# Kernel optimization log

Hardware: AMD Instinct MI355X
Metric: run time of the kernel (lower is better)

Reference implementation:

```python
import jax, jax.numpy as jnp
import numpy as np

N = 50000
E = 800000
IN_DIM = 128
H1 = 512
H2 = 300
OUT_DIM = 10
EPS = 1e-5


def setup_inputs() -> dict:
    key = jax.random.key(0)
    ks = jax.random.split(key, 12)
    x = jax.random.normal(ks[0], (N, IN_DIM), dtype=jnp.float32)
    edge_index = jax.random.randint(ks[1], (2, E), 0, N, dtype=jnp.int64)
    edge_weight = jax.random.uniform(ks[2], (E,), dtype=jnp.float32)
    def glorot(k, fan_in, fan_out):
        lim = np.sqrt(6.0 / (fan_in + fan_out)).astype(np.float32)
        return jax.random.uniform(k, (fan_in, fan_out), jnp.float32, -lim, lim)
    return {
        "x": x,
        "edge_index": edge_index,
        "edge_weight": edge_weight,
        "W1": glorot(ks[3], IN_DIM, H1), "b1": jnp.zeros((H1,), jnp.float32),
        "g1": jnp.ones((H1,), jnp.float32), "beta1": jnp.zeros((H1,), jnp.float32),
        "W2": glorot(ks[4], H1, H2), "b2": jnp.zeros((H2,), jnp.float32),
        "g2": jnp.ones((H2,), jnp.float32), "beta2": jnp.zeros((H2,), jnp.float32),
        "Wl": glorot(ks[5], H2, OUT_DIM), "bl": jnp.zeros((OUT_DIM,), jnp.float32),
    }


def _gcn_norm(edge_index, edge_weight, n):
    # add self loops (fill value 1.0), then symmetric normalization (PyG gcn_norm)
    si = jnp.arange(n, dtype=edge_index.dtype)
    row = jnp.concatenate([edge_index[0], si])  # source
    col = jnp.concatenate([edge_index[1], si])  # target
    w = jnp.concatenate([edge_weight, jnp.ones((n,), edge_weight.dtype)])
    deg = jax.ops.segment_sum(w, col, num_segments=n)
    dis = jnp.where(deg > 0, jax.lax.rsqrt(deg), 0.0)
    return row, col, dis[row] * w * dis[col]


def _propagate(h, row, col, norm, n):
    # gather source rows, weight, scatter-add into targets
    return jax.ops.segment_sum(h[row] * norm[:, None], col, num_segments=n)


def _batchnorm(h, g, beta):
    mean = jnp.mean(h, axis=0)
    var = jnp.mean(jnp.square(h - mean), axis=0)  # biased var (torch BN)
    return (h - mean) * jax.lax.rsqrt(var + EPS) * g + beta


def reference(x, edge_index, edge_weight, W1, b1, g1, beta1,
              W2, b2, g2, beta2, Wl, bl):
    n = x.shape[0]
    row, col, norm = _gcn_norm(edge_index, edge_weight, n)
    # layer 1: aggregate then transform (== GCNConv's lin-then-propagate math)
    h = _propagate(x, row, col, norm, n) @ W1 + b1
    h = jax.nn.relu(_batchnorm(h, g1, beta1))
    # layer 2: transform then aggregate
    h = _propagate(h @ W2, row, col, norm, n) + b2
    h = jax.nn.relu(_batchnorm(h, g2, beta2))
    # classifier head + log_softmax
    h = jax.nn.relu(h @ Wl + bl)
    return jax.nn.log_softmax(h, axis=1)
```

## Files before the change

### kernel.cpp

```cpp
#include <hip/hip_runtime.h>
#include <math.h>

namespace {

constexpr int kIn  = 128;
constexpr int kH1  = 512;
constexpr int kH2  = 300;
constexpr int kH2p = 304;
constexpr int kW2R = 384;
constexpr int kOut = 10;
constexpr float kEps = 1e-5f;

typedef __attribute__((ext_vector_type(8))) short bf16x8;
typedef __attribute__((ext_vector_type(4))) float f32x4;

__device__ __forceinline__ void atomAddF(float* p, float v) { unsafeAtomicAdd(p, v); }

__device__ __forceinline__ unsigned short f2bf(float f) {
  unsigned u = __builtin_bit_cast(unsigned, f);
  unsigned r = u + 0x7fffu + ((u >> 16) & 1u);
  return (unsigned short)(r >> 16);
}
__device__ __forceinline__ float bf2f(unsigned short h) {
  return __builtin_bit_cast(float, (unsigned)h << 16);
}
__device__ __forceinline__ float blo(unsigned u) { return __builtin_bit_cast(float, u << 16); }
__device__ __forceinline__ float bhi(unsigned u) { return __builtin_bit_cast(float, u & 0xffff0000u); }
__device__ __forceinline__ unsigned pk2(float a, float b) {
  return (unsigned)f2bf(a) | ((unsigned)f2bf(b) << 16);
}

__device__ __forceinline__ void gload16(const unsigned short* g, unsigned short* l) {
  __builtin_amdgcn_global_load_lds(
      (const __attribute__((address_space(1))) unsigned int*)g,
      (__attribute__((address_space(3))) unsigned int*)l, 16, 0, 0);
}

__device__ __forceinline__ void fma8(const uint4& q, float w, float* acc) {
  acc[0] = fmaf(blo(q.x), w, acc[0]);
  acc[1] = fmaf(bhi(q.x), w, acc[1]);
  acc[2] = fmaf(blo(q.y), w, acc[2]);
  acc[3] = fmaf(bhi(q.y), w, acc[3]);
  acc[4] = fmaf(blo(q.z), w, acc[4]);
  acc[5] = fmaf(bhi(q.z), w, acc[5]);
  acc[6] = fmaf(blo(q.w), w, acc[6]);
  acc[7] = fmaf(bhi(q.w), w, acc[7]);
}

__global__ void k_prep(float* __restrict__ deg, int* __restrict__ cnt,
                       const float* __restrict__ x, unsigned short* __restrict__ xbf,
                       float* __restrict__ st,
                       const float* __restrict__ W1, unsigned short* __restrict__ W1T,
                       const float* __restrict__ W2, unsigned short* __restrict__ W2T, int n) {
  int i = blockIdx.x * blockDim.x + threadIdx.x;
  if (i < n) { deg[i] = 1.0f; cnt[i] = 0; }
  if (i < 4096) st[i] = 0.f;
  if (i < kIn * kH1) {
    int nn = i / kIn, k = i - nn * kIn;
    W1T[i] = f2bf(W1[(size_t)k * kH1 + nn]);
  }
  if (i < kW2R * kH1) {
    int nn = i / kH1, k = i - nn * kH1;
    W2T[i] = (nn < kH2) ? f2bf(W2[(size_t)k * kH2 + nn]) : (unsigned short)0;
  }
  if (i < n * 16) {
    int node = i >> 4, g = i & 15;
    const float4* xp = reinterpret_cast<const float4*>(x + (size_t)node * kIn + g * 8);
    float4 v0 = xp[0], v1 = xp[1];
    uint4 o;
    o.x = pk2(v0.x, v0.y); o.y = pk2(v0.z, v0.w);
    o.z = pk2(v1.x, v1.y); o.w = pk2(v1.z, v1.w);
    reinterpret_cast<uint4*>(xbf)[i] = o;
  }
}

__global__ void k_deg_cnt(float* __restrict__ deg, int* __restrict__ cnt,
                          const int* __restrict__ ei, const float* __restrict__ w, int nE) {
  int i = blockIdx.x * blockDim.x + threadIdx.x;
  if (i < nE) {
    int c = ei[nE + i];
    atomAddF(&deg[c], w[i]);
    atomicAdd(&cnt[c], 1);
  }
}

__global__ void k_dis(float* __restrict__ deg, int n) {
  int i = blockIdx.x * blockDim.x + threadIdx.x;
  if (i < n) deg[i] = rsqrtf(deg[i]);
}

__global__ void k_scan_a(int* __restrict__ cnt, int* __restrict__ bsum, int n) {
  __shared__ int ws[4];
  int i = blockIdx.x * 256 + threadIdx.x;
  int lane = threadIdx.x & 63, wid = threadIdx.x >> 6;
  int v = (i < n) ? cnt[i] : 0;
  int s = v;
#pragma unroll
  for (int off = 1; off < 64; off <<= 1) {
    int t = __shfl_up(s, off);
    if (lane >= off) s += t;
  }
  if (lane == 63) ws[wid] = s;
  __syncthreads();
  int add = 0;
  if (wid > 0) add += ws[0];
  if (wid > 1) add += ws[1];
  if (wid > 2) add += ws[2];
  if (i < n) cnt[i] = s - v + add;
  if (threadIdx.x == 255) bsum[blockIdx.x] = add + s;
}

__global__ void k_scan_b(int* __restrict__ bsum, int nb) {
  __shared__ int ws[4];
  int i = threadIdx.x;
  int lane = i & 63, wid = i >> 6;
  int v = (i < nb) ? bsum[i] : 0;
  int s = v;
#pragma unroll
  for (int off = 1; off < 64; off <<= 1) {
    int t = __shfl_up(s, off);
    if (lane >= off) s += t;
  }
  if (lane == 63) ws[wid] = s;
  __syncthreads();
  int add = 0;
  if (wid > 0) add += ws[0];
  if (wid > 1) add += ws[1];
  if (wid > 2) add += ws[2];
  if (i < nb) bsum[i] = s - v + add;
}

__global__ void k_scan_c(int* __restrict__ cnt, const int* __restrict__ bsum, int n) {
  int i = blockIdx.x * 256 + threadIdx.x;
  if (i < n) cnt[i] += bsum[blockIdx.x];
}

__global__ void k_scatter(int* __restrict__ cnt, const int* __restrict__ ei,
                          const float* __restrict__ w, const float* __restrict__ dis,
                          uint2* __restrict__ pr, int nE) {
  int i = blockIdx.x * blockDim.x + threadIdx.x;
  if (i < nE) {
    int r = ei[i];
    int c = ei[nE + i];
    int pos = atomicAdd(&cnt[c], 1);
    float ww = dis[r] * w[i] * dis[c];
    pr[pos] = make_uint2((unsigned)r, __builtin_bit_cast(unsigned, ww));
  }
}

template<int NSQ>
__global__ void k_gather(const unsigned short* __restrict__ X, const int* __restrict__ endp,
                         const uint2* __restrict__ pr, const float* __restrict__ dis,
                         unsigned short* __restrict__ out, int n) {
  int tid = blockIdx.x * blockDim.x + threadIdx.x;
  int v = tid / NSQ;
  int s = tid - v * NSQ;
  if (v >= n) return;
  int beg = (v == 0) ? 0 : endp[v - 1];
  int end = endp[v];
  const uint4* Xr = reinterpret_cast<const uint4*>(X);
  float d = dis[v];
  float sw = d * d;
  float acc[8];
  {
    uint4 q = Xr[(size_t)v * NSQ + s];
    acc[0] = blo(q.x) * sw; acc[1] = bhi(q.x) * sw;
    acc[2] = blo(q.y) * sw; acc[3] = bhi(q.y) * sw;
    acc[4] = blo(q.z) * sw; acc[5] = bhi(q.z) * sw;
    acc[6] = blo(q.w) * sw; acc[7] = bhi(q.w) * sw;
  }
  int e = beg;
  for (; e + 4 <= end; e += 4) {
    uint2 p0 = pr[e], p1 = pr[e + 1], p2 = pr[e + 2], p3 = pr[e + 3];
    uint4 q0 = Xr[(size_t)p0.x * NSQ + s];
    uint4 q1 = Xr[(size_t)p1.x * NSQ + s];
    uint4 q2 = Xr[(size_t)p2.x * NSQ + s];
    uint4 q3 = Xr[(size_t)p3.x * NSQ + s];
    fma8(q0, __builtin_bit_cast(float, p0.y), acc);
    fma8(q1, __builtin_bit_cast(float, p1.y), acc);
    fma8(q2, __builtin_bit_cast(float, p2.y), acc);
    fma8(q3, __builtin_bit_cast(float, p3.y), acc);
  }
  for (; e < end; ++e) {
    uint2 p = pr[e];
    uint4 q = Xr[(size_t)p.x * NSQ + s];
    fma8(q, __builtin_bit_cast(float, p.y), acc);
  }
  uint4 o;
  o.x = pk2(acc[0], acc[1]);
  o.y = pk2(acc[2], acc[3]);
  o.z = pk2(acc[4], acc[5]);
  o.w = pk2(acc[6], acc[7]);
  reinterpret_cast<uint4*>(out)[(size_t)v * NSQ + s] = o;
}

__global__ __launch_bounds__(256) void k_gemm(const unsigned short* __restrict__ A,
    const unsigned short* __restrict__ BT, unsigned short* __restrict__ C,
    int M, int Nlog, int K, int ntiles, int nwg) {
  constexpr int BK = 64;
  __shared__ unsigned short lA[(BK / 8) * 128 * 8];
  __shared__ unsigned short lB[(BK / 8) * 128 * 8];

  int p = blockIdx.x;
  int xcd = p & 7, idx = p >> 3;
  int q8 = nwg >> 3, r8 = nwg & 7;
  int logical = (xcd < r8 ? xcd * (q8 + 1) : r8 * (q8 + 1) + (xcd - r8) * q8) + idx;
  const int nt = logical % ntiles;
  const int mt = logical / ntiles;
  const int m0 = mt * 128, n0 = nt * 128;

  const int tid = threadIdx.x, lane = tid & 63, wid = tid >> 6;
  const int wr = wid >> 1, wc = wid & 1;
  const int fr = lane & 15, fq = lane >> 4;

  int arow[4], brow[4], k8s[4];
#pragma unroll
  for (int j = 0; j < 4; ++j) {
    int g = tid + 256 * j;
    int row = g & 127;
    k8s[j] = g >> 7;
    int ar = m0 + row;
    arow[j] = (ar < M) ? ar : (M - 1);
    brow[j] = n0 + row;
  }

  f32x4 acc[4][4] = {};

  for (int k0 = 0; k0 < K; k0 += BK) {
    __syncthreads();
#pragma unroll
    for (int j = 0; j < 4; ++j) {
      int g = tid + 256 * j;
      gload16(A  + (size_t)arow[j] * K + k0 + k8s[j] * 8, &lA[g * 8]);
      gload16(BT + (size_t)brow[j] * K + k0 + k8s[j] * 8, &lB[g * 8]);
    }
    __syncthreads();
#pragma unroll
    for (int step = 0; step < 2; ++step) {
      bf16x8 af[4], bf[4];
#pragma unroll
      for (int m = 0; m < 4; ++m)
        af[m] = *reinterpret_cast<const bf16x8*>(
            &lA[(((step * 4 + fq) << 7) + wr * 64 + m * 16 + fr) * 8]);
#pragma unroll
      for (int nn = 0; nn < 4; ++nn)
        bf[nn] = *reinterpret_cast<const bf16x8*>(
            &lB[(((step * 4 + fq) << 7) + wc * 64 + nn * 16 + fr) * 8]);
#pragma unroll
      for (int m = 0; m < 4; ++m)
#pragma unroll
        for (int nn = 0; nn < 4; ++nn)
          acc[m][nn] = __builtin_amdgcn_mfma_f32_16x16x32_bf16(af[m], bf[nn], acc[m][nn], 0, 0, 0);
    }
  }

#pragma unroll
  for (int m = 0; m < 4; ++m) {
#pragma unroll
    for (int r = 0; r < 4; ++r) {
      int row = m0 + wr * 64 + m * 16 + fq * 4 + r;
      if (row >= M) continue;
#pragma unroll
      for (int nn = 0; nn < 4; ++nn) {
        int col = n0 + wc * 64 + nn * 16 + fr;
        if (col < Nlog)
          C[(size_t)row * Nlog + col] = f2bf(acc[m][nn][r]);
      }
    }
  }
}

template<int C>
__global__ __launch_bounds__(256) void k_bn_stats_co(const unsigned short* __restrict__ H,
                                                     float* __restrict__ s1, float* __restrict__ s2,
                                                     int n, int rpb) {
  constexpr int G = C / 8;
  __shared__ float redS[3][G][8];
  __shared__ float redQ[3][G][8];
  const int g = threadIdx.x & 63;
  const int rr = threadIdx.x >> 6;
  int r0 = blockIdx.x * rpb;
  int r1 = r0 + rpb; if (r1 > n) r1 = n;
  float sa[8] = {}, sq[8] = {};
  if (g < G) {
    for (int r = r0 + rr; r < r1; r += 4) {
      uint4 q = *reinterpret_cast<const uint4*>(H + (size_t)r * C + g * 8);
      float v[8] = {blo(q.x), bhi(q.x), blo(q.y), bhi(q.y),
                    blo(q.z), bhi(q.z), blo(q.w), bhi(q.w)};
#pragma unroll
      for (int j = 0; j < 8; ++j) {
        sa[j] += v[j];
        sq[j] = fmaf(v[j], v[j], sq[j]);
      }
    }
    if (rr > 0) {
#pragma unroll
      for (int j = 0; j < 8; ++j) {
        redS[rr - 1][g][j] = sa[j];
        redQ[rr - 1][g][j] = sq[j];
      }
    }
  }
  __syncthreads();
  if (rr == 0 && g < G) {
#pragma unroll
    for (int j = 0; j < 8; ++j) {
      float ts = sa[j] + redS[0][g][j] + redS[1][g][j] + redS[2][g][j];
      float tq = sq[j] + redQ[0][g][j] + redQ[1][g][j] + redQ[2][g][j];
      atomAddF(&s1[g * 8 + j], ts);
      atomAddF(&s2[g * 8 + j], tq);
    }
  }
}

__global__ void k_bn_finalize(const float* __restrict__ s1, const float* __restrict__ s2,
                              const float* __restrict__ g, const float* __restrict__ beta,
                              float* __restrict__ scale, float* __restrict__ shift,
                              int C, float invN) {
  int c = blockIdx.x * blockDim.x + threadIdx.x;
  if (c >= C) return;
  float mean = s1[c] * invN;
  float var = fmaxf(s2[c] * invN - mean * mean, 0.f);
  float sc = g[c] * rsqrtf(var + kEps);
  scale[c] = sc;
  shift[c] = beta[c] - mean * sc;
}

template<int C>
__global__ void k_bn_apply_relu_bf16(unsigned short* __restrict__ H,
                                     const float* __restrict__ scale,
                                     const float* __restrict__ shift, int total8) {
  int i = blockIdx.x * blockDim.x + threadIdx.x;
  if (i >= total8) return;
  uint4 q = reinterpret_cast<uint4*>(H)[i];
  int c = (i * 8) & (C - 1);
  unsigned w[4] = {q.x, q.y, q.z, q.w};
  unsigned o[4];
#pragma unroll
  for (int j = 0; j < 4; ++j) {
    float lo = blo(w[j]);
    float hi = bhi(w[j]);
    int cl = c + j * 2;
    lo = fmaxf(fmaf(lo, scale[cl],     shift[cl]),     0.f);
    hi = fmaxf(fmaf(hi, scale[cl + 1], shift[cl + 1]), 0.f);
    o[j] = pk2(lo, hi);
  }
  reinterpret_cast<uint4*>(H)[i] = make_uint4(o[0], o[1], o[2], o[3]);
}

__global__ __launch_bounds__(256) void k_head(const unsigned short* __restrict__ H,
    const float* __restrict__ scale, const float* __restrict__ shift,
    const float* __restrict__ Wl, const float* __restrict__ bl,
    float* __restrict__ out, int n) {
  __shared__ float sW[kH2 * kOut];
  __shared__ float sScale[kH2], sShift[kH2];
  for (int i = threadIdx.x; i < kH2 * kOut; i += blockDim.x) sW[i] = Wl[i];
  for (int i = threadIdx.x; i < kH2; i += blockDim.x) {
    sScale[i] = scale[i];
    sShift[i] = shift[i];
  }
  __syncthreads();
  float blv[kOut];
#pragma unroll
  for (int j = 0; j < kOut; ++j) blv[j] = bl[j];
  const int lane = threadIdx.x & 63;
  const int wid = (blockIdx.x * blockDim.x + threadIdx.x) >> 6;
  const int nw  = (gridDim.x * blockDim.x) >> 6;
  for (int node = wid; node < n; node += nw) {
    const unsigned short* hrow = H + (size_t)node * kH2p;
    float acc[kOut] = {};
    for (int k = lane; k < kH2; k += 64) {
      float v = fmaxf(fmaf(bf2f(hrow[k]), sScale[k], sShift[k]), 0.f);
      const float* wr = sW + k * kOut;
#pragma unroll
      for (int j = 0; j < kOut; ++j) acc[j] = fmaf(v, wr[j], acc[j]);
    }
#pragma unroll
    for (int j = 0; j < kOut; ++j) {
      float v = acc[j];
      for (int off = 32; off > 0; off >>= 1) v += __shfl_down(v, off);
      acc[j] = v;
    }
    if (lane == 0) {
      float vv[kOut], m = -1e30f;
#pragma unroll
      for (int j = 0; j < kOut; ++j) {
        vv[j] = fmaxf(acc[j] + blv[j], 0.f);
        m = fmaxf(m, vv[j]);
      }
      float s = 0.f;
#pragma unroll
      for (int j = 0; j < kOut; ++j) s += expf(vv[j] - m);
      float lse = m + logf(s);
      float* o = out + (size_t)node * kOut;
#pragma unroll
      for (int j = 0; j < kOut; ++j) o[j] = vv[j] - lse;
    }
  }
}

}

extern "C" void kernel_launch(void* const* d_in, const int* in_sizes, int n_in,
                              void* d_out, int out_size, void* d_ws, size_t ws_size,
                              hipStream_t stream) {
  const float* x   = (const float*)d_in[0];
  const int*   ei  = (const int*)d_in[1];
  const float* ew  = (const float*)d_in[2];
  const float* W1  = (const float*)d_in[3];
  const float* g1  = (const float*)d_in[5];
  const float* be1 = (const float*)d_in[6];
  const float* W2  = (const float*)d_in[7];
  const float* g2  = (const float*)d_in[9];
  const float* be2 = (const float*)d_in[10];
  const float* Wl  = (const float*)d_in[11];
  const float* bl  = (const float*)d_in[12];
  float* out = (float*)d_out;
  float* ws  = (float*)d_ws;

  const int n = in_sizes[0] / kIn;
  const int e = in_sizes[1] / 2;

  float* dis = ws;
  int*   cnt = (int*)(ws + 50048);
  uint2* pr  = (uint2*)(ws + 100096);
  float* st  = ws + 1700096;
  float* s1a = st,        *s2a = st + 512,  *sc1 = st + 1024, *sh1 = st + 1536;
  float* s1b = st + 2048, *s2b = st + 2560, *sc2 = st + 3072, *sh2 = st + 3584;
  int*   bsum = (int*)(ws + 1704192);
  unsigned short* xbf = (unsigned short*)(ws + 1704704);
  unsigned short* W1T = (unsigned short*)(ws + 4904704);
  unsigned short* W2T = (unsigned short*)(ws + 4937472);
  unsigned short* agg1 = (unsigned short*)(ws + 5035776);
  unsigned short* h1   = (unsigned short*)(ws + 8235776);
  unsigned short* t2   = (unsigned short*)(ws + 21035776);
  unsigned short* agg2 = (unsigned short*)(ws + 28635776);

  constexpr int TPB = 256;
  const int nb = (n + 255) / 256;
  const int rpb = (n + 255) / 256;

  k_prep<<<(n * 16 + TPB - 1) / TPB, TPB, 0, stream>>>(dis, cnt, x, xbf, st, W1, W1T, W2, W2T, n);
  k_deg_cnt<<<(e + TPB - 1) / TPB, TPB, 0, stream>>>(dis, cnt, ei, ew, e);
  k_dis<<<(n + TPB - 1) / TPB, TPB, 0, stream>>>(dis, n);
  k_scan_a<<<nb, 256, 0, stream>>>(cnt, bsum, n);
  k_scan_b<<<1, 256, 0, stream>>>(bsum, nb);
  k_scan_c<<<nb, 256, 0, stream>>>(cnt, bsum, n);
  k_scatter<<<(e + TPB - 1) / TPB, TPB, 0, stream>>>(cnt, ei, ew, dis, pr, e);

  const int mtiles = (n + 127) / 128;

  {
    int tot = n * (kIn / 8);
    k_gather<kIn / 8><<<(tot + TPB - 1) / TPB, TPB, 0, stream>>>(xbf, cnt, pr, dis, agg1, n);
  }
  {
    int ntiles = kH1 / 128;
    int nwg = mtiles * ntiles;
    k_gemm<<<nwg, 256, 0, stream>>>(agg1, W1T, h1, n, kH1, kIn, ntiles, nwg);
  }
  k_bn_stats_co<kH1><<<256, 256, 0, stream>>>(h1, s1a, s2a, n, rpb);
  k_bn_finalize<<<(kH1 + 255) / 256, 256, 0, stream>>>(s1a, s2a, g1, be1, sc1, sh1, kH1, 1.0f / n);
  k_bn_apply_relu_bf16<kH1><<<((n * (kH1 / 8)) + TPB - 1) / TPB, TPB, 0, stream>>>(
      h1, sc1, sh1, n * (kH1 / 8));

  {
    int ntiles = kW2R / 128;
    int nwg = mtiles * ntiles;
    k_gemm<<<nwg, 256, 0, stream>>>(h1, W2T, t2, n, kH2p, kH1, ntiles, nwg);
  }
  {
    int tot = n * (kH2p / 8);
    k_gather<kH2p / 8><<<(tot + TPB - 1) / TPB, TPB, 0, stream>>>(t2, cnt, pr, dis, agg2, n);
  }
  k_bn_stats_co<kH2p><<<256, 256, 0, stream>>>(agg2, s1b, s2b, n, rpb);
  k_bn_finalize<<<(kH2 + 255) / 256, 256, 0, stream>>>(s1b, s2b, g2, be2, sc2, sh2, kH2, 1.0f / n);

  k_head<<<1024, 256, 0, stream>>>(agg2, sc2, sh2, Wl, bl, out, n);
}
```

Measured before the change: 534.9 us.

## Fuse BN1 stats into GEMM epilogue, fold dis into scan, finalize into head

Layer-1 batchnorm sums and sums of squares are now accumulated in the GEMM epilogue, using shared-memory atomics per tile and then global atomics, in place of a separate stats kernel that re-read the whole h1 matrix. The rsqrt degree kernel is folded into the first scan pass, and the layer-2 BN finalize is computed inside the head kernel's shared-memory setup. This removes one full read of a large activation tensor and two small launches. In exchange it adds atomic contention on the 512 stat columns, and the stats are taken from fp32 accumulators instead of bf16-rounded values, so results can differ slightly.

```diff
diff --git a/kernel.cpp b/kernel.cpp
--- a/kernel.cpp
+++ b/kernel.cpp
@@ -84,15 +84,12 @@
   }
 }
 
-__global__ void k_dis(float* __restrict__ deg, int n) {
-  int i = blockIdx.x * blockDim.x + threadIdx.x;
-  if (i < n) deg[i] = rsqrtf(deg[i]);
-}
-
-__global__ void k_scan_a(int* __restrict__ cnt, int* __restrict__ bsum, int n) {
+__global__ void k_scan_a(int* __restrict__ cnt, int* __restrict__ bsum,
+                         float* __restrict__ deg, int n) {
   __shared__ int ws[4];
   int i = blockIdx.x * 256 + threadIdx.x;
   int lane = threadIdx.x & 63, wid = threadIdx.x >> 6;
+  if (i < n) deg[i] = rsqrtf(deg[i]);
   int v = (i < n) ? cnt[i] : 0;
   int s = v;
 #pragma unroll
@@ -194,12 +191,15 @@
   reinterpret_cast<uint4*>(out)[(size_t)v * NSQ + s] = o;
 }
 
+template<bool STATS>
 __global__ __launch_bounds__(256) void k_gemm(const unsigned short* __restrict__ A,
     const unsigned short* __restrict__ BT, unsigned short* __restrict__ C,
+    float* __restrict__ s1g, float* __restrict__ s2g,
     int M, int Nlog, int K, int ntiles, int nwg) {
   constexpr int BK = 64;
   __shared__ unsigned short lA[(BK / 8) * 128 * 8];
   __shared__ unsigned short lB[(BK / 8) * 128 * 8];
+  __shared__ float sS[128], sQ[128];
 
   int p = blockIdx.x;
   int xcd = p & 7, idx = p >> 3;
@@ -213,6 +213,10 @@
   const int wr = wid >> 1, wc = wid & 1;
   const int fr = lane & 15, fq = lane >> 4;
 
+  if constexpr (STATS) {
+    if (tid < 128) { sS[tid] = 0.f; sQ[tid] = 0.f; }
+  }
+
   int arow[4], brow[4], k8s[4];
 #pragma unroll
   for (int j = 0; j < 4; ++j) {
@@ -266,6 +270,36 @@
         if (col < Nlog)
           C[(size_t)row * Nlog + col] = f2bf(acc[m][nn][r]);
       }
+    }
+  }
+
+  if constexpr (STATS) {
+    float ps[4] = {}, pq[4] = {};
+#pragma unroll
+    for (int m = 0; m < 4; ++m) {
+#pragma unroll
+      for (int r = 0; r < 4; ++r) {
+        int row = m0 + wr * 64 + m * 16 + fq * 4 + r;
+        if (row < M) {
+#pragma unroll
+          for (int nn = 0; nn < 4; ++nn) {
+            float v = acc[m][nn][r];
+            ps[nn] += v;
+            pq[nn] = fmaf(v, v, pq[nn]);
+          }
+        }
+      }
+    }
+#pragma unroll
+    for (int nn = 0; nn < 4; ++nn) {
+      int cl = wc * 64 + nn * 16 + fr;
+      atomicAdd(&sS[cl], ps[nn]);
+      atomicAdd(&sQ[cl], pq[nn]);
+    }
+    __syncthreads();
+    if (tid < 128) {
+      atomAddF(&s1g[n0 + tid], sS[tid]);
+      atomAddF(&s2g[n0 + tid], sQ[tid]);
     }
   }
 }
@@ -349,15 +383,19 @@
 }
 
 __global__ __launch_bounds__(256) void k_head(const unsigned short* __restrict__ H,
-    const float* __restrict__ scale, const float* __restrict__ shift,
+    const float* __restrict__ s1, const float* __restrict__ s2,
+    const float* __restrict__ g2, const float* __restrict__ be2,
     const float* __restrict__ Wl, const float* __restrict__ bl,
-    float* __restrict__ out, int n) {
+    float* __restrict__ out, int n, float invN) {
   __shared__ float sW[kH2 * kOut];
   __shared__ float sScale[kH2], sShift[kH2];
   for (int i = threadIdx.x; i < kH2 * kOut; i += blockDim.x) sW[i] = Wl[i];
   for (int i = threadIdx.x; i < kH2; i += blockDim.x) {
-    sScale[i] = scale[i];
-    sShift[i] = shift[i];
+    float mean = s1[i] * invN;
+    float var = fmaxf(s2[i] * invN - mean * mean, 0.f);
+    float sc = g2[i] * rsqrtf(var + kEps);
+    sScale[i] = sc;
+    sShift[i] = be2[i] - mean * sc;
   }
   __syncthreads();
   float blv[kOut];
@@ -426,7 +464,7 @@
   uint2* pr  = (uint2*)(ws + 100096);
   float* st  = ws + 1700096;
   float* s1a = st,        *s2a = st + 512,  *sc1 = st + 1024, *sh1 = st + 1536;
-  float* s1b = st + 2048, *s2b = st + 2560, *sc2 = st + 3072, *sh2 = st + 3584;
+  float* s1b = st + 2048, *s2b = st + 2560;
   int*   bsum = (int*)(ws + 1704192);
   unsigned short* xbf = (unsigned short*)(ws + 1704704);
   unsigned short* W1T = (unsigned short*)(ws + 4904704);
@@ -442,8 +480,7 @@
 
   k_prep<<<(n * 16 + TPB - 1) / TPB, TPB, 0, stream>>>(dis, cnt, x, xbf, st, W1, W1T, W2, W2T, n);
   k_deg_cnt<<<(e + TPB - 1) / TPB, TPB, 0, stream>>>(dis, cnt, ei, ew, e);
-  k_dis<<<(n + TPB - 1) / TPB, TPB, 0, stream>>>(dis, n);
-  k_scan_a<<<nb, 256, 0, stream>>>(cnt, bsum, n);
+  k_scan_a<<<nb, 256, 0, stream>>>(cnt, bsum, dis, n);
   k_scan_b<<<1, 256, 0, stream>>>(bsum, nb);
   k_scan_c<<<nb, 256, 0, stream>>>(cnt, bsum, n);
   k_scatter<<<(e + TPB - 1) / TPB, TPB, 0, stream>>>(cnt, ei, ew, dis, pr, e);
@@ -457,9 +494,8 @@
   {
     int ntiles = kH1 / 128;
     int nwg = mtiles * ntiles;
-    k_gemm<<<nwg, 256, 0, stream>>>(agg1, W1T, h1, n, kH1, kIn, ntiles, nwg);
-  }
-  k_bn_stats_co<kH1><<<256, 256, 0, stream>>>(h1, s1a, s2a, n, rpb);
+    k_gemm<true><<<nwg, 256, 0, stream>>>(agg1, W1T, h1, s1a, s2a, n, kH1, kIn, ntiles, nwg);
+  }
   k_bn_finalize<<<(kH1 + 255) / 256, 256, 0, stream>>>(s1a, s2a, g1, be1, sc1, sh1, kH1, 1.0f / n);
   k_bn_apply_relu_bf16<kH1><<<((n * (kH1 / 8)) + TPB - 1) / TPB, TPB, 0, stream>>>(
       h1, sc1, sh1, n * (kH1 / 8));
@@ -467,14 +503,13 @@
   {
     int ntiles = kW2R / 128;
     int nwg = mtiles * ntiles;
-    k_gemm<<<nwg, 256, 0, stream>>>(h1, W2T, t2, n, kH2p, kH1, ntiles, nwg);
+    k_gemm<false><<<nwg, 256, 0, stream>>>(h1, W2T, t2, nullptr, nullptr, n, kH2p, kH1, ntiles, nwg);
   }
   {
     int tot = n * (kH2p / 8);
     k_gather<kH2p / 8><<<(tot + TPB - 1) / TPB, TPB, 0, stream>>>(t2, cnt, pr, dis, agg2, n);
   }
   k_bn_stats_co<kH2p><<<256, 256, 0, stream>>>(agg2, s1b, s2b, n, rpb);
-  k_bn_finalize<<<(kH2 + 255) / 256, 256, 0, stream>>>(s1b, s2b, g2, be2, sc2, sh2, kH2, 1.0f / n);
-
-  k_head<<<1024, 256, 0, stream>>>(agg2, sc2, sh2, Wl, bl, out, n);
-}
+
+  k_head<<<1024, 256, 0, stream>>>(agg2, s1b, s2b, g2, be2, Wl, bl, out, n, 1.0f / n);
+}
```

After: 485.0 us. 9.3% less time.
